# Optimization experiments

Hardware: AMD Instinct MI355X
Metric: run time of the kernel (lower is better)

Reference implementation:

```python
import jax, jax.numpy as jnp
import numpy as np

LATENT = 1024
RED = 4            # reduce_proj
GROUPS = 16
K = 3              # kernel_size
PAD = 1
REGIONS = 36
CPG = LATENT // GROUPS   # channels per group (in and out), = 64
NEG = 0.1                # LeakyReLU slope


def l2norm(x, axis=-1):
    # faithful to lavse l2norm: x / sqrt(sum(x^2)) with no eps
    return x / jnp.sqrt(jnp.sum(x * x, axis=axis, keepdims=True))


def leaky(x):
    return jnp.where(x > 0, x, NEG * x)


def setup_inputs() -> dict:
    key = jax.random.key(0)
    ks = jax.random.split(key, 7)
    Bi, Bc, T = 128, 32, 50
    img_embed = jax.random.normal(ks[0], (Bi, REGIONS, LATENT), jnp.float32)
    cap_embed = jax.random.normal(ks[1], (Bc, T, LATENT), jnp.float32)
    lens = jax.random.randint(ks[2], (Bc,), 1, T + 1)  # word counts in [1, T]
    qdim = LATENT // RED
    s1 = 1.0 / np.sqrt(LATENT)
    red_w = jax.random.uniform(ks[3], (LATENT, qdim), jnp.float32, -s1, s1)
    red_b = jax.random.uniform(ks[4], (qdim,), jnp.float32, -s1, s1)
    nw = LATENT * CPG * K  # out_channels * (in_channels // groups) * kernel_size
    s2 = 1.0 / np.sqrt(qdim)
    proj_w = jax.random.uniform(ks[5], (qdim, nw), jnp.float32, -s2, s2)
    proj_b = jax.random.uniform(ks[6], (nw,), jnp.float32, -s2, s2)
    return dict(img_embed=img_embed, cap_embed=cap_embed, lens=lens,
                red_w=red_w, red_b=red_b, proj_w=proj_w, proj_b=proj_b)


def reference(img_embed, cap_embed, lens, red_w, red_b, proj_w, proj_b):
    Bi = img_embed.shape[0]
    Bc, T, C = cap_embed.shape
    # masked mean over the first n_words of each caption -> (Bc, C)
    mask = (jnp.arange(T)[None, :] < lens[:, None]).astype(cap_embed.dtype)
    cap_repr = jnp.sum(cap_embed * mask[:, :, None], axis=1) / lens[:, None].astype(cap_embed.dtype)
    cap_act = leaky(cap_repr)                       # 'cap' gate, (Bc, C)
    # dynamic depthwise-grouped conv weights from reduced query
    q = cap_repr @ red_w + red_b                    # (Bc, qdim)
    w = (q @ proj_w + proj_b).reshape(Bc, LATENT, CPG, K)
    w = jax.nn.softmax(w, axis=-1)                  # weightnorm='softmax' over kernel dim
    w = w.reshape(Bc, GROUPS, CPG, CPG, K)          # (Bc, g, out/g, in/g, K)
    # grouped conv1d over 36 regions, padding=1
    img = img_embed.transpose(0, 2, 1)              # (Bi, C, L)
    imgp = jnp.pad(img, ((0, 0), (0, 0), (PAD, PAD)))
    shif = jnp.stack([imgp[:, :, k:k + REGIONS] for k in range(K)], axis=-1)  # (Bi, C, L, K)
    shif = shif.reshape(Bi, GROUPS, CPG, REGIONS, K)
    out = jnp.einsum('bgilk,ngoik->nbgol', shif, w).reshape(Bc, Bi, LATENT, REGIONS)
    out = leaky(out)
    # (x * cap).mean(-1) == x.mean(-1) * cap since cap broadcasts over positions
    img_vec = l2norm(jnp.mean(out, axis=-1) * cap_act[:, None, :])  # (Bc, Bi, C)
    cap_vec = l2norm(cap_repr)                                      # (Bc, C)
    sims = jnp.einsum('nbc,nc->bn', img_vec, cap_vec)               # (Bi, Bc)
    return sims
```

## Files before the change

kernel.cpp:

```cpp
#include <hip/hip_runtime.h>
#include <math.h>

#define LATENT 1024
#define QDIM 256
#define NW 196608
#define BI 128
#define BC 32
#define TT 50
#define REGIONS 36
#define NGROUPS 16
#define CPG 64
#define NEG 0.1f

typedef __attribute__((ext_vector_type(8))) short short8;
typedef __attribute__((ext_vector_type(16))) float f32x16;

__device__ __forceinline__ float leakyf(float x){ return x > 0.f ? x : NEG * x; }

__device__ __forceinline__ unsigned short f2bf(float x){
    union { float f; unsigned int u; } v; v.f = x;
    unsigned int r = v.u + 0x7FFFu + ((v.u >> 16) & 1u);
    return (unsigned short)(r >> 16);
}

__global__ __launch_bounds__(256) void cap_mean_kernel(
    const float* __restrict__ cap_embed, const int* __restrict__ lens,
    float* __restrict__ cap_repr, float* __restrict__ cap_act,
    float* __restrict__ norm_capr)
{
    const int n = blockIdx.x;
    const int len = lens[n];
    const float invl = 1.f / (float)len;
    const int c4 = threadIdx.x;
    const float* base = cap_embed + (size_t)n * TT * LATENT + c4 * 4;
    float4 s = {0.f, 0.f, 0.f, 0.f};
    for (int t = 0; t < len; ++t) {
        const float4 v = *reinterpret_cast<const float4*>(base + (size_t)t * LATENT);
        s.x += v.x; s.y += v.y; s.z += v.z; s.w += v.w;
    }
    float4 m = {s.x * invl, s.y * invl, s.z * invl, s.w * invl};
    *reinterpret_cast<float4*>(cap_repr + n * LATENT + c4 * 4) = m;
    const float sc = 1.f / 36.f;
    float4 a = {leakyf(m.x) * sc, leakyf(m.y) * sc, leakyf(m.z) * sc, leakyf(m.w) * sc};
    *reinterpret_cast<float4*>(cap_act + n * LATENT + c4 * 4) = a;
    float ss = m.x*m.x + m.y*m.y + m.z*m.z + m.w*m.w;
    #pragma unroll
    for (int off = 32; off; off >>= 1) ss += __shfl_xor(ss, off);
    __shared__ float red4[4];
    if ((threadIdx.x & 63) == 0) red4[threadIdx.x >> 6] = ss;
    __syncthreads();
    if (threadIdx.x == 0) norm_capr[n] = sqrtf(red4[0] + red4[1] + red4[2] + red4[3]);
}

__global__ __launch_bounds__(256) void q_kernel(
    const float* __restrict__ cap_repr, const float* __restrict__ red_w,
    const float* __restrict__ red_b, unsigned short* __restrict__ qbfF)
{
    const int cg = blockIdx.x, n = blockIdx.y;
    const int col = threadIdx.x & 31, ks = threadIdx.x >> 5;
    const float* cr = cap_repr + n * LATENT;
    float p = 0.f;
    const int r0 = ks * 128;
    for (int r = r0; r < r0 + 128; ++r)
        p = fmaf(cr[r], red_w[(size_t)r * QDIM + cg * 32 + col], p);
    __shared__ float part[256];
    part[threadIdx.x] = p;
    __syncthreads();
    if (threadIdx.x < 32) {
        float s = red_b[cg * 32 + col];
        #pragma unroll
        for (int k = 0; k < 8; ++k) s += part[k * 32 + col];
        const int r = cg * 32 + col;
        const int elem = (r >> 4) * 512 + ((r >> 3) & 1) * 256 + n * 8 + (r & 7);
        qbfF[elem] = f2bf(s);
    }
}

__global__ __launch_bounds__(512, 2) void wgen10nt_kernel(
    const unsigned short* __restrict__ qbfF, const float* __restrict__ proj_w,
    const float* __restrict__ proj_b, unsigned short* __restrict__ Wp2F)
{
    __shared__ float L[768 * 32];
    __shared__ float pbs[768];
    const int tid = threadIdx.x;
    const int bx = blockIdx.x;
    const int colbase = bx * 768;
    const int wv = tid >> 6, lane = tid & 63;
    const int lrow = lane & 31, khalf = lane >> 5;

    for (int i = tid; i < 768; i += 512) pbs[i] = proj_b[colbase + i];

    short8 qfr[16];
    {
        const unsigned short* qp = qbfF + (size_t)lane * 8;
        #pragma unroll
        for (int s = 0; s < 16; ++s)
            qfr[s] = *reinterpret_cast<const short8*>(qp + s * 512);
    }

    const float* pw0 = proj_w + (size_t)(khalf * 8) * NW + colbase + wv * 96 + lrow;
    const float* pw1 = pw0 + 32;
    const float* pw2 = pw0 + 64;

    float a0[8], a1[8], a2[8], b0[8], b1[8], b2[8];
    #pragma unroll
    for (int j = 0; j < 8; ++j) {
        a0[j] = __builtin_nontemporal_load(&pw0[(size_t)j * NW]);
        a1[j] = __builtin_nontemporal_load(&pw1[(size_t)j * NW]);
        a2[j] = __builtin_nontemporal_load(&pw2[(size_t)j * NW]);
    }

    f32x16 acc0 = {}, acc1 = {}, acc2 = {};
    #pragma unroll
    for (int s = 0; s < 16; ++s) {
        if (s < 15) {
            const size_t roff = (size_t)((s + 1) * 16) * NW;
            #pragma unroll
            for (int j = 0; j < 8; ++j) {
                b0[j] = __builtin_nontemporal_load(&pw0[roff + (size_t)j * NW]);
                b1[j] = __builtin_nontemporal_load(&pw1[roff + (size_t)j * NW]);
                b2[j] = __builtin_nontemporal_load(&pw2[roff + (size_t)j * NW]);
            }
        }
        unsigned short u0[8], u1[8], u2[8];
        #pragma unroll
        for (int j = 0; j < 8; ++j) {
            u0[j] = f2bf(a0[j]); u1[j] = f2bf(a1[j]); u2[j] = f2bf(a2[j]);
        }
        acc0 = __builtin_amdgcn_mfma_f32_32x32x16_bf16(*reinterpret_cast<const short8*>(u0), qfr[s], acc0, 0, 0, 0);
        acc1 = __builtin_amdgcn_mfma_f32_32x32x16_bf16(*reinterpret_cast<const short8*>(u1), qfr[s], acc1, 0, 0, 0);
        acc2 = __builtin_amdgcn_mfma_f32_32x32x16_bf16(*reinterpret_cast<const short8*>(u2), qfr[s], acc2, 0, 0, 0);
        #pragma unroll
        for (int j = 0; j < 8; ++j) { a0[j] = b0[j]; a1[j] = b1[j]; a2[j] = b2[j]; }
    }

    __syncthreads();
    #pragma unroll
    for (int reg = 0; reg < 16; ++reg) {
        const int rit = (reg & 3) + 8 * (reg >> 2) + 4 * khalf;
        const int c = wv * 96 + rit;
        L[c * 32 + lrow]        = acc0[reg] + pbs[c];
        L[(c + 32) * 32 + lrow] = acc1[reg] + pbs[c + 32];
        L[(c + 64) * 32 + lrow] = acc2[reg] + pbs[c + 64];
    }
    __syncthreads();

    const int g = bx >> 4;
    const int obase = (bx & 15) * 4;
    for (int idx = tid; idx < 8192; idx += 512) {
        const int n = idx & 31, i = idx >> 5;
        const int c = i * 3;
        const float x0 = L[c * 32 + n], x1 = L[(c+1)*32 + n], x2 = L[(c+2)*32 + n];
        const float m = fmaxf(fmaxf(x0, x1), x2);
        const float e0 = expf(x0 - m), e1 = expf(x1 - m), e2 = expf(x2 - m);
        const float inv = 1.f / (e0 + e1 + e2);
        const int o = obase + (i >> 6);
        const int ii = i & 63;
        const int nt = o >> 5, lrow_o = o & 31;
        const int ks = ii >> 4, kh = (ii >> 3) & 1, j = ii & 7;
        const size_t base = (size_t)(n * 16 + g) * 12288
                          + (size_t)(nt * 4 + ks) * 512
                          + kh * 256 + lrow_o * 8 + j;
        Wp2F[base]        = f2bf(e0 * inv);
        Wp2F[base + 4096] = f2bf(e1 * inv);
        Wp2F[base + 8192] = f2bf(e2 * inv);
    }
}

__global__ __launch_bounds__(576, 3) void conv5_kernel(
    const float* __restrict__ img_embed, const unsigned short* __restrict__ Wp2F,
    const float* __restrict__ cap_repr, const float* __restrict__ cap_act,
    float* __restrict__ part_dot, float* __restrict__ part_ss)
{
    const int g = blockIdx.x, bt = blockIdx.y, nq = blockIdx.z;
    const int b0 = bt * 8;
    __shared__ int4 BsmV[3072];
    char* BsmRaw = (char*)BsmV;
    __shared__ float Sw[2][9][2][64];
    const int tid = threadIdx.x;
    const int wv = tid >> 6, lane = tid & 63;
    const int lrow = lane & 31, khalf = lane >> 5;
    const int ioff = khalf * 16;

    const float* imgG = img_embed + (size_t)b0 * 36 * 1024 + g * 64;
    for (int idx = tid; idx < 2304; idx += 576) {
        const int row_img = idx >> 3, ch = idx & 7;
        const int bbs = row_img / 36;
        const int l = row_img - bbs * 36;
        const float* src = imgG + (size_t)row_img * 1024 + ch * 8;
        const float4 u = *reinterpret_cast<const float4*>(src);
        const float4 v = *reinterpret_cast<const float4*>(src + 4);
        unsigned short r8[8];
        r8[0]=f2bf(u.x); r8[1]=f2bf(u.y); r8[2]=f2bf(u.z); r8[3]=f2bf(u.w);
        r8[4]=f2bf(v.x); r8[5]=f2bf(v.y); r8[6]=f2bf(v.z); r8[7]=f2bf(v.w);
        const int arow = bbs * 38 + l + 1;
        const int byte = (arow * 128 + ch * 16) ^ ((arow & 7) << 4);
        *reinterpret_cast<int4*>(BsmRaw + byte) = *reinterpret_cast<const int4*>(r8);
    }
    if (tid < 128) {
        const int rr = tid >> 3, ch = tid & 7;
        const int arow = (rr >> 1) * 38 + (rr & 1) * 37;
        const int byte = (arow * 128 + ch * 16) ^ ((arow & 7) << 4);
        int4 z; z.x = 0; z.y = 0; z.z = 0; z.w = 0;
        *reinterpret_cast<int4*>(BsmRaw + byte) = z;
    }
    __syncthreads();

    const int rg = wv * 32 + lrow;
    const int bbr = rg / 36;
    const int abase = bbr * 38 + (rg - bbr * 36);
    short8 afr[3][4];
    #pragma unroll
    for (int k = 0; k < 3; ++k)
        #pragma unroll
        for (int ks = 0; ks < 4; ++ks) {
            const int arow = abase + k;
            const int byte = (arow * 128 + ks * 32 + ioff) ^ ((arow & 7) << 4);
            afr[k][ks] = *reinterpret_cast<const short8*>(BsmRaw + byte);
        }
    const int rbase = wv * 32;
    const int bfirst = rbase / 36;
    const int bsplit = (bfirst + 1) * 36 - rbase;
    __syncthreads();

    const int n0 = nq * 16;
    int4 st0, st1, st2;
    {
        const unsigned short* WF = Wp2F + (size_t)(n0 * 16 + g) * 12288;
        st0 = *reinterpret_cast<const int4*>(WF + (size_t)tid * 8);
        st1 = *reinterpret_cast<const int4*>(WF + (size_t)(tid + 576) * 8);
        if (tid < 384) st2 = *reinterpret_cast<const int4*>(WF + (size_t)(tid + 1152) * 8);
        *reinterpret_cast<int4*>(BsmRaw + (size_t)tid * 16) = st0;
        *reinterpret_cast<int4*>(BsmRaw + (size_t)(tid + 576) * 16) = st1;
        if (tid < 384) *reinterpret_cast<int4*>(BsmRaw + (size_t)(tid + 1152) * 16) = st2;
    }
    __syncthreads();

    for (int ni = 0; ni < 16; ++ni) {
        const int n = n0 + ni;
        char* Bcur = BsmRaw + (size_t)(ni & 1) * 24576;
        char* Bnxt = BsmRaw + (size_t)((ni + 1) & 1) * 24576;

        if (ni < 15) {
            const unsigned short* WF = Wp2F + (size_t)((n + 1) * 16 + g) * 12288;
            st0 = *reinterpret_cast<const int4*>(WF + (size_t)tid * 8);
            st1 = *reinterpret_cast<const int4*>(WF + (size_t)(tid + 576) * 8);
            if (tid < 384) st2 = *reinterpret_cast<const int4*>(WF + (size_t)(tid + 1152) * 8);
        }

        f32x16 acc0 = {}, acc1 = {};
        #pragma unroll
        for (int k = 0; k < 3; ++k) {
            #pragma unroll
            for (int ks = 0; ks < 4; ++ks) {
                const char* fb = Bcur + k * 8192 + ks * 1024 + (size_t)lane * 16;
                const short8 bf0 = *reinterpret_cast<const short8*>(fb);
                const short8 bf1 = *reinterpret_cast<const short8*>(fb + 4096);
                acc0 = __builtin_amdgcn_mfma_f32_32x32x16_bf16(afr[k][ks], bf0, acc0, 0, 0, 0);
                acc1 = __builtin_amdgcn_mfma_f32_32x32x16_bf16(afr[k][ks], bf1, acc1, 0, 0, 0);
            }
        }

        if (ni < 15) {
            *reinterpret_cast<int4*>(Bnxt + (size_t)tid * 16) = st0;
            *reinterpret_cast<int4*>(Bnxt + (size_t)(tid + 576) * 16) = st1;
            if (tid < 384) *reinterpret_cast<int4*>(Bnxt + (size_t)(tid + 1152) * 16) = st2;
        }

        float s0A = 0.f, s0B = 0.f, s1A = 0.f, s1B = 0.f;
        #pragma unroll
        for (int reg = 0; reg < 16; ++reg) {
            const int rit = (reg & 3) + 8 * (reg >> 2) + 4 * khalf;
            const float v0 = leakyf(acc0[reg]);
            const float v1 = leakyf(acc1[reg]);
            if (rit >= bsplit) { s0B += v0; s1B += v1; }
            else               { s0A += v0; s1A += v1; }
        }
        s0A += __shfl_xor(s0A, 32); s0B += __shfl_xor(s0B, 32);
        s1A += __shfl_xor(s1A, 32); s1B += __shfl_xor(s1B, 32);
        const int q = ni & 1;
        if (khalf == 0) {
            Sw[q][wv][0][lrow]      = s0A;
            Sw[q][wv][0][32 + lrow] = s1A;
            if (bsplit < 32) {
                Sw[q][wv][1][lrow]      = s0B;
                Sw[q][wv][1][32 + lrow] = s1B;
            }
        }
        __syncthreads();

        if (tid < 128) {
            const int b = tid >> 4, j = tid & 15;
            const float4 ca4 = *reinterpret_cast<const float4*>(&cap_act [n * LATENT + g * CPG + j * 4]);
            const float4 cr4 = *reinterpret_cast<const float4*>(&cap_repr[n * LATENT + g * CPG + j * 4]);
            const float cav[4] = {ca4.x, ca4.y, ca4.z, ca4.w};
            const float crv[4] = {cr4.x, cr4.y, cr4.z, cr4.w};
            float d = 0.f, ss = 0.f;
            #pragma unroll
            for (int u = 0; u < 4; ++u) {
                const int o = j * 4 + u;
                const float S = (b == 0)
                    ? Sw[q][0][0][o] + Sw[q][1][0][o]
                    : Sw[q][b][1][o] + Sw[q][b + 1][0][o];
                const float tmp = S * cav[u];
                d = fmaf(tmp, crv[u], d);
                ss = fmaf(tmp, tmp, ss);
            }
            #pragma unroll
            for (int off = 1; off <= 8; off <<= 1) {
                d += __shfl_xor(d, off);
                ss += __shfl_xor(ss, off);
            }
            if (j == 0) {
                part_dot[((size_t)n * BI + b0 + b) * NGROUPS + g] = d;
                part_ss [((size_t)n * BI + b0 + b) * NGROUPS + g] = ss;
            }
        }
    }
}

__global__ __launch_bounds__(256) void final_kernel(
    const float* __restrict__ part_dot, const float* __restrict__ part_ss,
    const float* __restrict__ norm_capr, float* __restrict__ out)
{
    const int idx = blockIdx.x * 256 + threadIdx.x;
    const int n = idx & 31;
    const int b = idx >> 5;
    const size_t base = ((size_t)n * BI + b) * NGROUPS;
    float d = 0.f, s = 0.f;
    #pragma unroll
    for (int g = 0; g < NGROUPS; ++g) { d += part_dot[base + g]; s += part_ss[base + g]; }
    out[b * BC + n] = d / (sqrtf(s) * norm_capr[n]);
}

extern "C" void kernel_launch(void* const* d_in, const int* in_sizes, int n_in,
                              void* d_out, int out_size, void* d_ws, size_t ws_size,
                              hipStream_t stream) {
    const float* img_embed = (const float*)d_in[0];
    const float* cap_embed = (const float*)d_in[1];
    const int*   lens      = (const int*)  d_in[2];
    const float* red_w     = (const float*)d_in[3];
    const float* red_b     = (const float*)d_in[4];
    const float* proj_w    = (const float*)d_in[5];
    const float* proj_b    = (const float*)d_in[6];
    float* out = (float*)d_out;

    char* ws = (char*)d_ws;
    unsigned short* Wp2F   = (unsigned short*)(ws);
    float* cap_repr  = (float*)(ws + 22020096);
    float* cap_act   = (float*)(ws + 22151168);
    unsigned short* qbfF = (unsigned short*)(ws + 22282240);
    float* norm_capr = (float*)(ws + 22315008);
    float* part_dot  = (float*)(ws + 22315520);
    float* part_ss   = (float*)(ws + 22577664);

    hipLaunchKernelGGL(cap_mean_kernel, dim3(BC), dim3(256), 0, stream,
                       cap_embed, lens, cap_repr, cap_act, norm_capr);
    hipLaunchKernelGGL(q_kernel, dim3(8, BC), dim3(256), 0, stream,
                       cap_repr, red_w, red_b, qbfF);
    hipLaunchKernelGGL(wgen10nt_kernel, dim3(256), dim3(512), 0, stream,
                       qbfF, proj_w, proj_b, Wp2F);
    hipLaunchKernelGGL(conv5_kernel, dim3(NGROUPS, 16, 2), dim3(576), 0, stream,
                       img_embed, Wp2F, cap_repr, cap_act, part_dot, part_ss);
    hipLaunchKernelGGL(final_kernel, dim3(16), dim3(256), 0, stream,
                       part_dot, part_ss, norm_capr, out);
}
```

Before: 179.1 us.

## Stage proj_w through LDS with float4 loads and transposed bf16 reads

```diff
diff --git a/kernel.cpp b/kernel.cpp
--- a/kernel.cpp
+++ b/kernel.cpp
@@ -23,6 +23,12 @@
     return (unsigned short)(r >> 16);
 }
 
+__device__ __forceinline__ unsigned long long pack4(float4 v){
+    unsigned int lo = (unsigned int)f2bf(v.x) | ((unsigned int)f2bf(v.y) << 16);
+    unsigned int hi = (unsigned int)f2bf(v.z) | ((unsigned int)f2bf(v.w) << 16);
+    return (unsigned long long)lo | ((unsigned long long)hi << 32);
+}
+
 __global__ __launch_bounds__(256) void cap_mean_kernel(
     const float* __restrict__ cap_embed, const int* __restrict__ lens,
     float* __restrict__ cap_repr, float* __restrict__ cap_act,
@@ -76,78 +82,102 @@
     }
 }
 
-__global__ __launch_bounds__(512, 2) void wgen10nt_kernel(
+__global__ __launch_bounds__(768, 3) void wgen13_kernel(
     const unsigned short* __restrict__ qbfF, const float* __restrict__ proj_w,
     const float* __restrict__ proj_b, unsigned short* __restrict__ Wp2F)
 {
+    __shared__ unsigned short Stg[24576];
     __shared__ float L[768 * 32];
     __shared__ float pbs[768];
-    const int tid = threadIdx.x;
-    const int bx = blockIdx.x;
+    const int tid = threadIdx.x, bx = blockIdx.x;
     const int colbase = bx * 768;
     const int wv = tid >> 6, lane = tid & 63;
     const int lrow = lane & 31, khalf = lane >> 5;
-
-    for (int i = tid; i < 768; i += 512) pbs[i] = proj_b[colbase + i];
+    const int wcol = wv * 64;
+
+    pbs[tid] = proj_b[colbase + tid];
 
     short8 qfr[16];
     {
         const unsigned short* qp = qbfF + (size_t)lane * 8;
         #pragma unroll
-        for (int s = 0; s < 16; ++s)
-            qfr[s] = *reinterpret_cast<const short8*>(qp + s * 512);
-    }
-
-    const float* pw0 = proj_w + (size_t)(khalf * 8) * NW + colbase + wv * 96 + lrow;
-    const float* pw1 = pw0 + 32;
-    const float* pw2 = pw0 + 64;
-
-    float a0[8], a1[8], a2[8], b0[8], b1[8], b2[8];
-    #pragma unroll
-    for (int j = 0; j < 8; ++j) {
-        a0[j] = __builtin_nontemporal_load(&pw0[(size_t)j * NW]);
-        a1[j] = __builtin_nontemporal_load(&pw1[(size_t)j * NW]);
-        a2[j] = __builtin_nontemporal_load(&pw2[(size_t)j * NW]);
-    }
-
-    f32x16 acc0 = {}, acc1 = {}, acc2 = {};
+        for (int s = 0; s < 16; ++s) qfr[s] = *reinterpret_cast<const short8*>(qp + s * 512);
+    }
+
+    const int sc4 = lane & 15;
+    const int rsub = lane >> 4;
+    const float* gsrc = proj_w + colbase + wcol + sc4 * 4 + (size_t)rsub * NW;
+    const int ew = (sc4 >> 2) * 64 + rsub * 16 + (sc4 & 3) * 4;
+    unsigned short* wbase = &Stg[wv * 2048];
+
+    const unsigned int stg0 = (unsigned int)(size_t)(void*)Stg + wv * 4096;
+    const unsigned int et0 = ((khalf * 8 + 0 + (lrow >> 4)) * 64 + (lrow & 15)) * 2;
+    const unsigned int et1 = ((khalf * 8 + 2 + (lrow >> 4)) * 64 + (lrow & 15)) * 2;
+
+    float4 gA[4], gB[4];
+    #pragma unroll
+    for (int i = 0; i < 4; ++i)
+        gA[i] = *reinterpret_cast<const float4*>(gsrc + (size_t)(i * 4) * NW);
+    #pragma unroll
+    for (int i = 0; i < 4; ++i)
+        gB[i] = *reinterpret_cast<const float4*>(gsrc + (size_t)(16 + i * 4) * NW);
+    #pragma unroll
+    for (int i = 0; i < 4; ++i)
+        *reinterpret_cast<unsigned long long*>(&wbase[ew + i * 256]) = pack4(gA[i]);
+
+    f32x16 acc0 = {}, acc1 = {};
     #pragma unroll
     for (int s = 0; s < 16; ++s) {
         if (s < 15) {
-            const size_t roff = (size_t)((s + 1) * 16) * NW;
-            #pragma unroll
-            for (int j = 0; j < 8; ++j) {
-                b0[j] = __builtin_nontemporal_load(&pw0[roff + (size_t)j * NW]);
-                b1[j] = __builtin_nontemporal_load(&pw1[roff + (size_t)j * NW]);
-                b2[j] = __builtin_nontemporal_load(&pw2[roff + (size_t)j * NW]);
-            }
-        }
-        unsigned short u0[8], u1[8], u2[8];
-        #pragma unroll
-        for (int j = 0; j < 8; ++j) {
-            u0[j] = f2bf(a0[j]); u1[j] = f2bf(a1[j]); u2[j] = f2bf(a2[j]);
-        }
-        acc0 = __builtin_amdgcn_mfma_f32_32x32x16_bf16(*reinterpret_cast<const short8*>(u0), qfr[s], acc0, 0, 0, 0);
-        acc1 = __builtin_amdgcn_mfma_f32_32x32x16_bf16(*reinterpret_cast<const short8*>(u1), qfr[s], acc1, 0, 0, 0);
-        acc2 = __builtin_amdgcn_mfma_f32_32x32x16_bf16(*reinterpret_cast<const short8*>(u2), qfr[s], acc2, 0, 0, 0);
-        #pragma unroll
-        for (int j = 0; j < 8; ++j) { a0[j] = b0[j]; a1[j] = b1[j]; a2[j] = b2[j]; }
+            if (((s + 1) & 1) == 1) {
+                #pragma unroll
+                for (int i = 0; i < 4; ++i)
+                    *reinterpret_cast<unsigned long long*>(&wbase[1024 + ew + i * 256]) = pack4(gB[i]);
+                if (s < 14) {
+                    #pragma unroll
+                    for (int i = 0; i < 4; ++i)
+                        gB[i] = *reinterpret_cast<const float4*>(gsrc + (size_t)((s + 2) * 16 + i * 4) * NW);
+                }
+            } else {
+                #pragma unroll
+                for (int i = 0; i < 4; ++i)
+                    *reinterpret_cast<unsigned long long*>(&wbase[ew + i * 256]) = pack4(gA[i]);
+                if (s < 14) {
+                    #pragma unroll
+                    for (int i = 0; i < 4; ++i)
+                        gA[i] = *reinterpret_cast<const float4*>(gsrc + (size_t)((s + 2) * 16 + i * 4) * NW);
+                }
+            }
+        }
+
+        unsigned long long t00, t01, t10, t11;
+        const unsigned int ab = stg0 + (unsigned int)((s & 1) * 2048);
+        asm volatile("ds_read_b64_tr_b16 %0, %1" : "=v"(t00) : "v"(ab + et0) : "memory");
+        asm volatile("ds_read_b64_tr_b16 %0, %1 offset:512" : "=v"(t01) : "v"(ab + et0) : "memory");
+        asm volatile("ds_read_b64_tr_b16 %0, %1" : "=v"(t10) : "v"(ab + et1) : "memory");
+        asm volatile("ds_read_b64_tr_b16 %0, %1 offset:512" : "=v"(t11) : "v"(ab + et1) : "memory");
+        asm volatile("s_waitcnt lgkmcnt(0)" ::: "memory");
+        __builtin_amdgcn_sched_barrier(0);
+        union U { unsigned long long u[2]; short8 v; };
+        U u0; u0.u[0] = t00; u0.u[1] = t01;
+        U u1; u1.u[0] = t10; u1.u[1] = t11;
+        acc0 = __builtin_amdgcn_mfma_f32_32x32x16_bf16(u0.v, qfr[s], acc0, 0, 0, 0);
+        acc1 = __builtin_amdgcn_mfma_f32_32x32x16_bf16(u1.v, qfr[s], acc1, 0, 0, 0);
     }
 
     __syncthreads();
     #pragma unroll
     for (int reg = 0; reg < 16; ++reg) {
         const int rit = (reg & 3) + 8 * (reg >> 2) + 4 * khalf;
-        const int c = wv * 96 + rit;
-        L[c * 32 + lrow]        = acc0[reg] + pbs[c];
-        L[(c + 32) * 32 + lrow] = acc1[reg] + pbs[c + 32];
-        L[(c + 64) * 32 + lrow] = acc2[reg] + pbs[c + 64];
+        const int c0 = wcol + rit, c1 = wcol + 32 + rit;
+        L[c0 * 32 + lrow] = acc0[reg] + pbs[c0];
+        L[c1 * 32 + lrow] = acc1[reg] + pbs[c1];
     }
     __syncthreads();
 
     const int g = bx >> 4;
     const int obase = (bx & 15) * 4;
-    for (int idx = tid; idx < 8192; idx += 512) {
+    for (int idx = tid; idx < 8192; idx += 768) {
         const int n = idx & 31, i = idx >> 5;
         const int c = i * 3;
         const float x0 = L[c * 32 + n], x1 = L[(c+1)*32 + n], x2 = L[(c+2)*32 + n];
@@ -358,7 +388,7 @@
                        cap_embed, lens, cap_repr, cap_act, norm_capr);
     hipLaunchKernelGGL(q_kernel, dim3(8, BC), dim3(256), 0, stream,
                        cap_repr, red_w, red_b, qbfF);
-    hipLaunchKernelGGL(wgen10nt_kernel, dim3(256), dim3(512), 0, stream,
+    hipLaunchKernelGGL(wgen13_kernel, dim3(256), dim3(768), 0, stream,
                        qbfF, proj_w, proj_b, Wp2F);
     hipLaunchKernelGGL(conv5_kernel, dim3(NGROUPS, 16, 2), dim3(576), 0, stream,
                        img_embed, Wp2F, cap_repr, cap_act, part_dot, part_ss);
```

Result: faster. 174.6 us (median of 2 runs) (-2.5%).
